# Kernel optimization log

Measured on AMD Instinct MI355X. Metric: run time of the kernel, lower is better.

## Reference

```python
import jax, jax.numpy as jnp
import numpy as np

B, S, D, H = 2, 2048, 2048, 16
HD = D // H
ROPE_BASE = 10000.0
N_DOCS = 8


def setup_inputs() -> dict:
    key = jax.random.key(0)
    ks = jax.random.split(key, 7)
    scale = 1.0 / np.sqrt(D)
    x = jax.random.normal(ks[0], (B, S, D), dtype=jnp.float32)
    doc_ids = jnp.sort(jax.random.randint(ks[1], (B, S), 0, N_DOCS), axis=1)
    Wq = jax.random.normal(ks[2], (D, D), dtype=jnp.float32) * scale
    Wk = jax.random.normal(ks[3], (D, D), dtype=jnp.float32) * scale
    Wv = jax.random.normal(ks[4], (D, D), dtype=jnp.float32) * scale
    Wo = jax.random.normal(ks[5], (D, D), dtype=jnp.float32) * scale
    bo = jax.random.normal(ks[6], (D,), dtype=jnp.float32) * 0.01
    return {"x": x, "doc_ids": doc_ids, "Wq": Wq, "Wk": Wk, "Wv": Wv, "Wo": Wo, "bo": bo}


def _rotate_half(t):
    # interleaved pairs: (x0,x1,x2,x3,...) -> (-x1,x0,-x3,x2,...)
    t1 = t[..., 0::2]
    t2 = t[..., 1::2]
    return jnp.stack((-t2, t1), axis=-1).reshape(t.shape)


def _doc_position_ids(doc_ids):
    b, s = doc_ids.shape
    boundary = jnp.concatenate(
        [jnp.ones((b, 1), dtype=bool), doc_ids[:, 1:] != doc_ids[:, :-1]], axis=1)
    ar = jnp.arange(s)[None, :]
    boundary_pos = jnp.where(boundary, ar, 0)
    last_boundary = jax.lax.cummax(boundary_pos, axis=1)
    return ar - last_boundary  # position within each document


def reference(x, doc_ids, Wq, Wk, Wv, Wo, bo):
    b, s, d = x.shape
    h, hd = H, HD

    q = (x @ Wq).reshape(b, s, h, hd).transpose(0, 2, 1, 3)  # [b,h,s,hd]
    k = (x @ Wk).reshape(b, s, h, hd).transpose(0, 2, 1, 3)
    v = (x @ Wv).reshape(b, s, h, hd).transpose(0, 2, 1, 3)

    # doc-aware RoPE: positions reset at document boundaries
    pos = _doc_position_ids(doc_ids).astype(jnp.float32)  # [b,s]
    inv_freq = 1.0 / (ROPE_BASE ** (jnp.arange(0, hd, 2, dtype=jnp.float32) / hd))
    freqs = pos[..., None] * inv_freq  # [b,s,hd/2]
    cos = jnp.repeat(jnp.cos(freqs), 2, axis=-1)[:, None]  # [b,1,s,hd]
    sin = jnp.repeat(jnp.sin(freqs), 2, axis=-1)[:, None]
    q = q * cos + _rotate_half(q) * sin
    k = k * cos + _rotate_half(k) * sin

    scores = jnp.einsum("bhqd,bhkd->bhqk", q, k)
    # doc-blockwise causal mask: attend only to j<=i within same document
    same_doc = doc_ids[:, :, None] == doc_ids[:, None, :]  # [b,s,s] (i,j)
    allowed = jnp.tril(same_doc)[:, None]  # [b,1,s,s]
    inv_scale = 1.0 / np.sqrt(hd)
    scores = jnp.where(allowed, scores * inv_scale, -jnp.inf)
    attn = jax.nn.softmax(scores, axis=-1)

    ctx = jnp.einsum("bhqk,bhkd->bhqd", attn, v)
    ctx = ctx.transpose(0, 2, 1, 3).reshape(b, s, d)
    return ctx @ Wo + bo
```

## Files before the change

### kernel.cpp

```cpp
#include <hip/hip_runtime.h>
#include <hip/hip_bf16.h>

#define Dd 2048
#define Ss 2048
#define Bb 2
#define Hh 16
#define HDd 128
#define BSs (Bb*Ss)
#define NTIL 32

typedef __bf16 bf16;
typedef __bf16 bf16x8 __attribute__((ext_vector_type(8)));
typedef __bf16 bf16x4 __attribute__((ext_vector_type(4)));
typedef float f32x4 __attribute__((ext_vector_type(4)));

__device__ __forceinline__ void gload_lds16(const void* g, void* l) {
  __builtin_amdgcn_global_load_lds((__attribute__((address_space(1))) void*)(g),
                                   (__attribute__((address_space(3))) void*)(l), 16, 0, 0);
}

template <int N>
__device__ __forceinline__ void waitv() {
  if constexpr (N == 0) asm volatile("s_waitcnt vmcnt(0)" ::: "memory");
  else if constexpr (N == 6) asm volatile("s_waitcnt vmcnt(6)" ::: "memory");
}

__global__ void k_cvtx(const float* __restrict__ x, bf16* __restrict__ xb) {
  int i = (blockIdx.x * 256 + threadIdx.x) * 4;
  f32x4 v = *(const f32x4*)(x + i);
  bf16x4 o;
  o[0] = (bf16)v[0]; o[1] = (bf16)v[1]; o[2] = (bf16)v[2]; o[3] = (bf16)v[3];
  *(bf16x4*)(xb + i) = o;
}

__global__ void k_tw(const float* __restrict__ W0, const float* __restrict__ W1,
                     const float* __restrict__ W2, const float* __restrict__ W3,
                     bf16* __restrict__ T0, bf16* __restrict__ T1,
                     bf16* __restrict__ T2, bf16* __restrict__ T3) {
  const float* W; bf16* T;
  switch (blockIdx.z) {
    case 0: W = W0; T = T0; break;
    case 1: W = W1; T = T1; break;
    case 2: W = W2; T = T2; break;
    default: W = W3; T = T3; break;
  }
  __shared__ float t[64][65];
  int n0 = blockIdx.x * 64, k0 = blockIdx.y * 64;
  int tid = threadIdx.x;
#pragma unroll
  for (int rr = 0; rr < 4; rr++) {
    int r = (tid >> 4) + rr * 16;
    f32x4 vv = *(const f32x4*)(W + (size_t)(k0 + r) * Dd + n0 + (tid & 15) * 4);
#pragma unroll
    for (int j = 0; j < 4; j++) t[r][(tid & 15) * 4 + j] = vv[j];
  }
  __syncthreads();
#pragma unroll
  for (int rr = 0; rr < 4; rr++) {
    int n = rr * 16 + (tid >> 4);
    int kb = (tid & 15) * 4;
    bf16x4 o;
#pragma unroll
    for (int j = 0; j < 4; j++) o[j] = (bf16)t[kb + j][n];
    *(bf16x4*)(T + (size_t)(n0 + n) * Dd + k0 + kb) = o;
  }
}

__global__ void k_pos(const int* __restrict__ doc, int* __restrict__ pos) {
  int b = blockIdx.x;
  __shared__ int bp[2][Ss];
  const int* db = doc + (size_t)b * Ss;
  for (int i = threadIdx.x; i < Ss; i += 1024) {
    int bd = (i == 0) || (db[i] != db[i - 1]);
    bp[0][i] = bd ? i : 0;
  }
  __syncthreads();
  int src = 0;
  for (int off = 1; off < Ss; off <<= 1) {
    for (int i = threadIdx.x; i < Ss; i += 1024) {
      int v = bp[src][i];
      if (i >= off) v = max(v, bp[src][i - off]);
      bp[1 - src][i] = v;
    }
    __syncthreads();
    src = 1 - src;
  }
  for (int i = threadIdx.x; i < Ss; i += 1024)
    pos[(size_t)b * Ss + i] = i - bp[src][i];
}

__device__ __forceinline__ void stage64(const char* gA, const char* gB,
                                        int m0, int n0, int t, int buf,
                                        char* AL, char* BL, int tid) {
  int ktb = t * 128;
#pragma unroll
  for (int p = 0; p < 2; p++) {
    int o = p * 8192 + tid * 16;
    int r = o >> 7, cb = o & 127;
    gload_lds16(gA + (size_t)(m0 + r) * 4096 + ktb + (cb ^ ((r & 7) << 4)),
                AL + buf * 16384 + o);
  }
#pragma unroll
  for (int p = 0; p < 4; p++) {
    int o = p * 8192 + tid * 16;
    int r = o >> 7, cb = o & 127;
    gload_lds16(gB + (size_t)(n0 + r) * 4096 + ktb + (cb ^ ((r & 7) << 4)),
                BL + buf * 32768 + o);
  }
}

template <bool STAGE, int WV>
__device__ __forceinline__ void do_tile64(const char* gA, const char* gB, int m0, int n0,
                                          int t, int bi, int b2, char* AL, char* BL, int tid,
                                          int wr, int wc, int ln, int g,
                                          f32x4 (&acc)[4][4]) {
  if (STAGE) stage64(gA, gB, m0, n0, t + 2, b2, AL, BL, tid);
  const char* tA = AL + bi * 16384;
  const char* tB = BL + bi * 32768;
#pragma unroll
  for (int kk = 0; kk < 2; kk++) {
    bf16x8 af[4], bf[4];
#pragma unroll
    for (int mq = 0; mq < 4; mq++) {
      int row = wr * 64 + mq * 16 + ln;
      af[mq] = *(const bf16x8*)(tA + row * 128 + ((kk * 64 + g * 16) ^ ((row & 7) << 4)));
    }
#pragma unroll
    for (int nq = 0; nq < 4; nq++) {
      int row = wc * 64 + nq * 16 + ln;
      bf[nq] = *(const bf16x8*)(tB + row * 128 + ((kk * 64 + g * 16) ^ ((row & 7) << 4)));
    }
    __builtin_amdgcn_s_setprio(1);
#pragma unroll
    for (int mq = 0; mq < 4; mq++)
#pragma unroll
      for (int nq = 0; nq < 4; nq++)
        acc[mq][nq] = __builtin_amdgcn_mfma_f32_16x16x32_bf16(af[mq], bf[nq], acc[mq][nq], 0, 0, 0);
    __builtin_amdgcn_s_setprio(0);
  }
  waitv<WV>();
  __builtin_amdgcn_s_barrier();
}

__device__ __forceinline__ void gemm64_core(const bf16* gA_, const bf16* gB_,
                                            int m0, int n0, char* AL, char* BL,
                                            f32x4 (&acc)[4][4]) {
  const char* gA = (const char*)gA_;
  const char* gB = (const char*)gB_;
  const int tid = threadIdx.x;
  const int l = tid & 63, w = tid >> 6;
  const int wr = w >> 2, wc = w & 3;
  const int g = l >> 4, ln = l & 15;
  f32x4 z = {0.f, 0.f, 0.f, 0.f};
#pragma unroll
  for (int i = 0; i < 4; i++)
#pragma unroll
    for (int n = 0; n < 4; n++) acc[i][n] = z;

  stage64(gA, gB, m0, n0, 0, 0, AL, BL, tid);
  stage64(gA, gB, m0, n0, 1, 1, AL, BL, tid);
  waitv<6>();
  __builtin_amdgcn_s_barrier();

  for (int tt = 0; tt < 10; tt++) {
    int t = tt * 3;
    do_tile64<true, 6>(gA, gB, m0, n0, t,     0, 2, AL, BL, tid, wr, wc, ln, g, acc);
    do_tile64<true, 6>(gA, gB, m0, n0, t + 1, 1, 0, AL, BL, tid, wr, wc, ln, g, acc);
    do_tile64<true, 6>(gA, gB, m0, n0, t + 2, 2, 1, AL, BL, tid, wr, wc, ln, g, acc);
  }
  do_tile64<false, 0>(gA, gB, m0, n0, 30, 0, 0, AL, BL, tid, wr, wc, ln, g, acc);
  do_tile64<false, -1>(gA, gB, m0, n0, 31, 1, 0, AL, BL, tid, wr, wc, ln, g, acc);
}

__global__ __launch_bounds__(512, 2) void k_qkv256(const bf16* __restrict__ xb,
                                                   const bf16* __restrict__ wqkvt,
                                                   const int* __restrict__ pos,
                                                   bf16* __restrict__ q,
                                                   bf16* __restrict__ k,
                                                   bf16* __restrict__ vt) {
  __shared__ char SLM[147456];
  char* AL = SLM;
  char* BL = SLM + 49152;
  int bid = blockIdx.x;
  int x = bid & 7, j = bid >> 3;
  int mt = j / 3, nt = x * 3 + (j % 3);
  int m0 = mt * 128, n0 = nt * 256;

  f32x4 acc[4][4];
  gemm64_core(xb, wqkvt, m0, n0, AL, BL, acc);

  const int tid = threadIdx.x;
  const int l = tid & 63, w = tid >> 6;
  const int wr = w >> 2, wc = w & 3, g = l >> 4, ln = l & 15;
  int z = n0 >> 11;
  int n0l = n0 & 2047;
  int bix = m0 >> 11;
  int sl0 = m0 & 2047;

  if (z == 2) {
#pragma unroll
    for (int mq = 0; mq < 4; mq++) {
      int sl = sl0 + wr * 64 + mq * 16 + g * 4;
#pragma unroll
      for (int nq = 0; nq < 4; nq++) {
        int col = n0l + wc * 64 + nq * 16 + ln;
        int h = col >> 7, hd = col & 127;
        bf16x4 o;
#pragma unroll
        for (int r2 = 0; r2 < 4; r2++) o[r2] = (bf16)acc[mq][nq][r2];
        *(bf16x4*)(vt + (((size_t)(bix * Hh + h) * HDd + hd) * Ss + sl)) = o;
      }
    }
  } else {
    bf16* dst = (z == 0) ? q : k;
    float* T = (float*)SLM;
    const float c1 = 0.14391156642398168f;
    int cg = (tid & 31) * 8;
    int hb = n0l + cg;
    int hh = hb >> 7, hd0 = hb & 127;
    float fr[4];
#pragma unroll
    for (int pr = 0; pr < 4; pr++)
      fr[pr] = __expf(-(float)((hd0 >> 1) + pr) * c1);

#pragma unroll
    for (int pass = 0; pass < 2; pass++) {
      __syncthreads();
      if (wr == pass) {
#pragma unroll
        for (int mq = 0; mq < 4; mq++) {
#pragma unroll
          for (int nq = 0; nq < 4; nq++) {
            int c = wc * 64 + nq * 16 + ln;
            int rb = mq * 16 + g * 4;
#pragma unroll
            for (int r2 = 0; r2 < 4; r2++)
              T[(rb + r2) * 260 + c] = acc[mq][nq][r2];
          }
        }
      }
      __syncthreads();
#pragma unroll
      for (int j2 = 0; j2 < 4; j2++) {
        int r = j2 * 16 + (tid >> 5);
        int sg = m0 + pass * 64 + r;
        float p = (float)pos[sg];
        f32x4 v0 = *(const f32x4*)(T + r * 260 + cg);
        f32x4 v1 = *(const f32x4*)(T + r * 260 + cg + 4);
        float e0[4] = {v0[0], v0[2], v1[0], v1[2]};
        float e1[4] = {v0[1], v0[3], v1[1], v1[3]};
        int s = sg & 2047;
        bf16x8 o;
#pragma unroll
        for (int pr = 0; pr < 4; pr++) {
          float ang = p * fr[pr];
          float sn, cs;
          __sincosf(ang, &sn, &cs);
          o[2 * pr]     = (bf16)(e0[pr] * cs - e1[pr] * sn);
          o[2 * pr + 1] = (bf16)(e1[pr] * cs + e0[pr] * sn);
        }
        *(bf16x8*)(dst + (((size_t)(bix * Hh + hh) * Ss + s) * HDd + hd0)) = o;
      }
    }
  }
}

__global__ __launch_bounds__(512, 2) void k_out256(const bf16* __restrict__ ctx,
                                                   const bf16* __restrict__ wot,
                                                   const float* __restrict__ bo,
                                                   float* __restrict__ outp) {
  __shared__ char AL[49152];
  __shared__ char BL[98304];
  int bid = blockIdx.x;
  int x = bid & 7, j = bid >> 3;
  int mt = j, nt = x;
  int m0 = mt * 128, n0 = nt * 256;

  f32x4 acc[4][4];
  gemm64_core(ctx, wot, m0, n0, AL, BL, acc);

  const int l = threadIdx.x & 63, w = threadIdx.x >> 6;
  const int wr = w >> 2, wc = w & 3, g = l >> 4, ln = l & 15;
  float bov[4];
#pragma unroll
  for (int nq = 0; nq < 4; nq++)
    bov[nq] = bo[n0 + wc * 64 + nq * 16 + ln];
#pragma unroll
  for (int mq = 0; mq < 4; mq++)
#pragma unroll
    for (int r2 = 0; r2 < 4; r2++) {
      int row = m0 + wr * 64 + mq * 16 + g * 4 + r2;
#pragma unroll
      for (int nq = 0; nq < 4; nq++) {
        int col = n0 + wc * 64 + nq * 16 + ln;
        outp[(size_t)row * Dd + col] = acc[mq][nq][r2] + bov[nq];
      }
    }
}

__global__ __launch_bounds__(256) void k_attn(const bf16* __restrict__ q,
                                              const bf16* __restrict__ k,
                                              const bf16* __restrict__ vt,
                                              const int* __restrict__ pos,
                                              bf16* __restrict__ ctx) {
  __shared__ bf16 Ks[64 * 128];
  __shared__ bf16 Vts[128 * 64];
  __shared__ bf16 Pw[4][16 * 64];
  int bid = blockIdx.x;
  int xc = bid & 7, jj = bid >> 3;
  int bh = xc * 4 + (jj >> 5);
  int qt = jj & 31;
  int b = bh >> 4, h = bh & 15;
  int q0 = qt * 64;
  const int tid = threadIdx.x, l = tid & 63, w = tid >> 6, g = l >> 4, ln = l & 15;
  const bf16* qb = q + (size_t)bh * Ss * HDd;
  const bf16* kb = k + (size_t)bh * Ss * HDd;
  const bf16* vb = vt + (size_t)bh * Ss * HDd;

  bf16x8 qf[4];
  int qr = q0 + w * 16 + ln;
#pragma unroll
  for (int ks = 0; ks < 4; ks++)
    qf[ks] = *(const bf16x8*)(qb + (size_t)qr * HDd + ks * 32 + 8 * g);

  int rrow[4], dstart[4];
  float m[4], lsum[4];
#pragma unroll
  for (int r2 = 0; r2 < 4; r2++) {
    rrow[r2] = q0 + w * 16 + 4 * g + r2;
    dstart[r2] = rrow[r2] - pos[(size_t)b * Ss + rrow[r2]];
    m[r2] = -1e30f;
    lsum[r2] = 0.f;
  }
  f32x4 oacc[8];
  f32x4 z = {0.f, 0.f, 0.f, 0.f};
#pragma unroll
  for (int n = 0; n < 8; n++) oacc[n] = z;

  int kt_start = (q0 - pos[(size_t)b * Ss + q0]) >> 6;
  const float iscale = 0.08838834764831845f;

  for (int kt = kt_start; kt <= qt; kt++) {
    int kv0 = kt * 64;
#pragma unroll
    for (int i2 = 0; i2 < 4; i2++) {
      int o = i2 * 4096 + w * 1024 + l * 16;
      int rk = o >> 8, cbk = o & 255;
      gload_lds16((const char*)kb + (size_t)(kv0 + rk) * 256 + cbk,
                  (char*)Ks + i2 * 4096 + w * 1024);
      int rv = o >> 7, cbv = o & 127;
      gload_lds16((const char*)vb + (size_t)rv * (Ss * 2) + (size_t)kv0 * 2 + cbv,
                  (char*)Vts + i2 * 4096 + w * 1024);
    }
    __syncthreads();

    f32x4 sc[4];
#pragma unroll
    for (int n = 0; n < 4; n++) {
      f32x4 a = z;
#pragma unroll
      for (int ks = 0; ks < 4; ks++) {
        bf16x8 bfrag = *(const bf16x8*)(Ks + (n * 16 + ln) * 128 + ks * 32 + 8 * g);
        a = __builtin_amdgcn_mfma_f32_16x16x32_bf16(qf[ks], bfrag, a, 0, 0, 0);
      }
      sc[n] = a;
    }

    float pmax[4] = {-1e30f, -1e30f, -1e30f, -1e30f};
    float pv[4][4];
#pragma unroll
    for (int n = 0; n < 4; n++) {
      int kvc = kv0 + n * 16 + ln;
#pragma unroll
      for (int r2 = 0; r2 < 4; r2++) {
        bool ok = (kvc <= rrow[r2]) && (kvc >= dstart[r2]);
        float sv = ok ? sc[n][r2] * iscale : -1e30f;
        pv[n][r2] = sv;
        pmax[r2] = fmaxf(pmax[r2], sv);
      }
    }
#pragma unroll
    for (int off = 1; off < 16; off <<= 1)
#pragma unroll
      for (int r2 = 0; r2 < 4; r2++)
        pmax[r2] = fmaxf(pmax[r2], __shfl_xor(pmax[r2], off, 64));

    float alpha[4];
#pragma unroll
    for (int r2 = 0; r2 < 4; r2++) {
      float mn = fmaxf(m[r2], pmax[r2]);
      alpha[r2] = __expf(m[r2] - mn);
      m[r2] = mn;
    }

    float rs[4] = {0.f, 0.f, 0.f, 0.f};
#pragma unroll
    for (int n = 0; n < 4; n++) {
      int kvc = kv0 + n * 16 + ln;
#pragma unroll
      for (int r2 = 0; r2 < 4; r2++) {
        bool ok = (kvc <= rrow[r2]) && (kvc >= dstart[r2]);
        float p = ok ? __expf(pv[n][r2] - m[r2]) : 0.f;
        rs[r2] += p;
        Pw[w][(4 * g + r2) * 64 + n * 16 + ln] = (bf16)p;
      }
    }
#pragma unroll
    for (int off = 1; off < 16; off <<= 1)
#pragma unroll
      for (int r2 = 0; r2 < 4; r2++) rs[r2] += __shfl_xor(rs[r2], off, 64);
#pragma unroll
    for (int r2 = 0; r2 < 4; r2++) lsum[r2] = lsum[r2] * alpha[r2] + rs[r2];
#pragma unroll
    for (int n = 0; n < 8; n++)
#pragma unroll
      for (int r2 = 0; r2 < 4; r2++) oacc[n][r2] *= alpha[r2];
    __syncthreads();

#pragma unroll
    for (int n = 0; n < 8; n++) {
#pragma unroll
      for (int ks = 0; ks < 2; ks++) {
        bf16x8 pa = *(const bf16x8*)(&Pw[w][ln * 64 + ks * 32 + 8 * g]);
        bf16x8 vfr = *(const bf16x8*)(Vts + (n * 16 + ln) * 64 + ks * 32 + 8 * g);
        oacc[n] = __builtin_amdgcn_mfma_f32_16x16x32_bf16(pa, vfr, oacc[n], 0, 0, 0);
      }
    }
    __syncthreads();
  }

#pragma unroll
  for (int n = 0; n < 8; n++)
#pragma unroll
    for (int r2 = 0; r2 < 4; r2++) {
      float val = oacc[n][r2] / lsum[r2];
      ctx[((size_t)(b * Ss + rrow[r2])) * Dd + h * HDd + n * 16 + ln] = (bf16)val;
    }
}

extern "C" void kernel_launch(void* const* d_in, const int* in_sizes, int n_in,
                              void* d_out, int out_size, void* d_ws, size_t ws_size,
                              hipStream_t stream) {
  const float* x = (const float*)d_in[0];
  const int* doc = (const int*)d_in[1];
  const float* Wq = (const float*)d_in[2];
  const float* Wk = (const float*)d_in[3];
  const float* Wv = (const float*)d_in[4];
  const float* Wo = (const float*)d_in[5];
  const float* bo = (const float*)d_in[6];
  float* outp = (float*)d_out;

  char* ws = (char*)d_ws;
  size_t off = 0;
  auto alloc = [&](size_t bytes) {
    char* p = ws + off;
    off += (bytes + 255) & ~(size_t)255;
    return p;
  };
  bf16* xb = (bf16*)alloc((size_t)BSs * Dd * 2);
  bf16* wqkvt = (bf16*)alloc((size_t)3 * Dd * Dd * 2);
  bf16* wot = (bf16*)alloc((size_t)Dd * Dd * 2);
  bf16* qd = (bf16*)alloc((size_t)BSs * Dd * 2);
  bf16* kd = (bf16*)alloc((size_t)BSs * Dd * 2);
  bf16* vtd = (bf16*)alloc((size_t)BSs * Dd * 2);
  bf16* ctxd = (bf16*)alloc((size_t)BSs * Dd * 2);
  int* pos = (int*)alloc((size_t)BSs * 4);

  k_cvtx<<<(BSs * Dd) / 1024, 256, 0, stream>>>(x, xb);
  k_tw<<<dim3(Dd / 64, Dd / 64, 4), 256, 0, stream>>>(
      Wq, Wk, Wv, Wo, wqkvt, wqkvt + (size_t)Dd * Dd, wqkvt + (size_t)2 * Dd * Dd, wot);
  k_pos<<<Bb, 1024, 0, stream>>>(doc, pos);
  k_qkv256<<<dim3(768), 512, 0, stream>>>(xb, wqkvt, pos, qd, kd, vtd);
  k_attn<<<dim3(1024), 256, 0, stream>>>(qd, kd, vtd, pos, ctxd);
  k_out256<<<dim3(256), 512, 0, stream>>>(ctxd, wot, bo, outp);
}
```

Baseline: 220.3 us.

## Use 256x384 per-head QKV GEMM tiles with interleaved weight layout

```diff
diff --git a/kernel.cpp b/kernel.cpp
--- a/kernel.cpp
+++ b/kernel.cpp
@@ -33,19 +33,15 @@
   *(bf16x4*)(xb + i) = o;
 }
 
-__global__ void k_tw(const float* __restrict__ W0, const float* __restrict__ W1,
-                     const float* __restrict__ W2, const float* __restrict__ W3,
-                     bf16* __restrict__ T0, bf16* __restrict__ T1,
-                     bf16* __restrict__ T2, bf16* __restrict__ T3) {
-  const float* W; bf16* T;
-  switch (blockIdx.z) {
-    case 0: W = W0; T = T0; break;
-    case 1: W = W1; T = T1; break;
-    case 2: W = W2; T = T2; break;
-    default: W = W3; T = T3; break;
-  }
+__global__ void k_tw(const float* __restrict__ Wq, const float* __restrict__ Wk,
+                     const float* __restrict__ Wv, const float* __restrict__ Wo,
+                     bf16* __restrict__ wqkvt, bf16* __restrict__ wot) {
+  int zz = blockIdx.z;
+  const float* W = (zz == 0) ? Wq : (zz == 1) ? Wk : (zz == 2) ? Wv : Wo;
+  bf16* T = (zz < 3) ? wqkvt : wot;
   __shared__ float t[64][65];
   int n0 = blockIdx.x * 64, k0 = blockIdx.y * 64;
+  int trow0 = (zz < 3) ? ((n0 >> 7) * 384 + zz * 128 + (n0 & 127)) : n0;
   int tid = threadIdx.x;
 #pragma unroll
   for (int rr = 0; rr < 4; rr++) {
@@ -62,7 +58,7 @@
     bf16x4 o;
 #pragma unroll
     for (int j = 0; j < 4; j++) o[j] = (bf16)t[kb + j][n];
-    *(bf16x4*)(T + (size_t)(n0 + n) * Dd + k0 + kb) = o;
+    *(bf16x4*)(T + (size_t)(trow0 + n) * Dd + k0 + kb) = o;
   }
 }
 
@@ -87,6 +83,175 @@
   }
   for (int i = threadIdx.x; i < Ss; i += 1024)
     pos[(size_t)b * Ss + i] = i - bp[src][i];
+}
+
+__device__ __forceinline__ void stage384(const char* gA, const char* gB,
+                                         int m0, int n0, int t, int buf,
+                                         char* AL, char* BL, int tid) {
+  int ktb = t * 128;
+#pragma unroll
+  for (int p = 0; p < 4; p++) {
+    int o = p * 8192 + tid * 16;
+    int r = o >> 7, cb = o & 127;
+    gload_lds16(gA + (size_t)(m0 + r) * 4096 + ktb + (cb ^ ((r & 7) << 4)),
+                AL + buf * 32768 + o);
+  }
+#pragma unroll
+  for (int p = 0; p < 6; p++) {
+    int o = p * 8192 + tid * 16;
+    int r = o >> 7, cb = o & 127;
+    gload_lds16(gB + (size_t)(n0 + r) * 4096 + ktb + (cb ^ ((r & 7) << 4)),
+                BL + buf * 49152 + o);
+  }
+}
+
+template <bool STAGE, int WV>
+__device__ __forceinline__ void do_tile384(const char* gA, const char* gB, int m0, int n0,
+                                           int t, int bi, char* AL, char* BL, int tid,
+                                           int wr, int wc, int ln, int g,
+                                           f32x4 (&acc)[8][6]) {
+  if (STAGE) stage384(gA, gB, m0, n0, t + 1, bi ^ 1, AL, BL, tid);
+  const char* tA = AL + bi * 32768;
+  const char* tB = BL + bi * 49152;
+#pragma unroll
+  for (int kk = 0; kk < 2; kk++) {
+    bf16x8 bf[6];
+#pragma unroll
+    for (int nq = 0; nq < 6; nq++) {
+      int row = wc * 96 + nq * 16 + ln;
+      bf[nq] = *(const bf16x8*)(tB + row * 128 + ((kk * 64 + g * 16) ^ ((row & 7) << 4)));
+    }
+#pragma unroll
+    for (int mh = 0; mh < 2; mh++) {
+      bf16x8 af[4];
+#pragma unroll
+      for (int mq = 0; mq < 4; mq++) {
+        int row = wr * 128 + mh * 64 + mq * 16 + ln;
+        af[mq] = *(const bf16x8*)(tA + row * 128 + ((kk * 64 + g * 16) ^ ((row & 7) << 4)));
+      }
+      __builtin_amdgcn_s_setprio(1);
+#pragma unroll
+      for (int mq = 0; mq < 4; mq++)
+#pragma unroll
+        for (int nq = 0; nq < 6; nq++)
+          acc[mh * 4 + mq][nq] =
+              __builtin_amdgcn_mfma_f32_16x16x32_bf16(af[mq], bf[nq], acc[mh * 4 + mq][nq], 0, 0, 0);
+      __builtin_amdgcn_s_setprio(0);
+    }
+  }
+  waitv<WV>();
+  if (WV >= 0) __builtin_amdgcn_s_barrier();
+}
+
+__global__ __launch_bounds__(512, 2) void k_qkv384(const bf16* __restrict__ xb,
+                                                   const bf16* __restrict__ wqkvt,
+                                                   const int* __restrict__ pos,
+                                                   bf16* __restrict__ q,
+                                                   bf16* __restrict__ k,
+                                                   bf16* __restrict__ vt) {
+  __shared__ char SLM[163840];
+  char* AL = SLM;
+  char* BL = SLM + 65536;
+  int bid = blockIdx.x;
+  int x = bid & 7, j = bid >> 3;
+  int nt = x * 2 + (j >> 4);
+  int mt = j & 15;
+  int m0 = mt * 256, n0 = nt * 384;
+
+  const int tid = threadIdx.x;
+  const int l = tid & 63, w = tid >> 6;
+  const int wr = w >> 2, wc = w & 3;
+  const int g = l >> 4, ln = l & 15;
+
+  f32x4 acc[8][6];
+  f32x4 z = {0.f, 0.f, 0.f, 0.f};
+#pragma unroll
+  for (int i = 0; i < 8; i++)
+#pragma unroll
+    for (int n = 0; n < 6; n++) acc[i][n] = z;
+
+  const char* gA = (const char*)xb;
+  const char* gB = (const char*)wqkvt;
+  stage384(gA, gB, m0, n0, 0, 0, AL, BL, tid);
+  waitv<0>();
+  __builtin_amdgcn_s_barrier();
+  for (int t = 0; t < NTIL - 1; t++)
+    do_tile384<true, 0>(gA, gB, m0, n0, t, t & 1, AL, BL, tid, wr, wc, ln, g, acc);
+  do_tile384<false, -1>(gA, gB, m0, n0, NTIL - 1, (NTIL - 1) & 1, AL, BL, tid, wr, wc, ln, g, acc);
+
+  int h = nt;
+  int bix = m0 >> 11;
+  int sl0 = m0 & 2047;
+
+#pragma unroll
+  for (int mq = 0; mq < 8; mq++) {
+    int sl = sl0 + wr * 128 + mq * 16 + g * 4;
+#pragma unroll
+    for (int nq = 0; nq < 6; nq++) {
+      int cb0 = wc * 96 + nq * 16;
+      if (cb0 >= 256) {
+        int hd = cb0 - 256 + ln;
+        bf16x4 o;
+#pragma unroll
+        for (int r2 = 0; r2 < 4; r2++) o[r2] = (bf16)acc[mq][nq][r2];
+        *(bf16x4*)(vt + (((size_t)(bix * Hh + h) * HDd + hd) * Ss + sl)) = o;
+      }
+    }
+  }
+
+  float* T = (float*)SLM;
+  const float c1 = 0.14391156642398168f;
+  int cg = (tid & 31) * 8;
+  int zz = cg >> 7;
+  int hd0 = cg & 127;
+  bf16* dst = (zz == 0) ? q : k;
+  float fr[4];
+#pragma unroll
+  for (int pr = 0; pr < 4; pr++)
+    fr[pr] = __expf(-(float)((hd0 >> 1) + pr) * c1);
+
+#pragma unroll
+  for (int pass = 0; pass < 4; pass++) {
+    __syncthreads();
+    if (wr == (pass >> 1)) {
+#pragma unroll
+      for (int mq2 = 0; mq2 < 4; mq2++) {
+        int mq = (pass & 1) * 4 + mq2;
+#pragma unroll
+        for (int nq = 0; nq < 6; nq++) {
+          int cb0 = wc * 96 + nq * 16;
+          if (cb0 < 256) {
+            int rb = mq2 * 16 + g * 4;
+#pragma unroll
+            for (int r2 = 0; r2 < 4; r2++)
+              T[(rb + r2) * 260 + cb0 + ln] = acc[mq][nq][r2];
+          }
+        }
+      }
+    }
+    __syncthreads();
+#pragma unroll
+    for (int j2 = 0; j2 < 4; j2++) {
+      int r = j2 * 16 + (tid >> 5);
+      int sg = m0 + pass * 64 + r;
+      float p = (float)pos[sg];
+      f32x4 v0 = *(const f32x4*)(T + r * 260 + cg);
+      f32x4 v1 = *(const f32x4*)(T + r * 260 + cg + 4);
+      float e0[4] = {v0[0], v0[2], v1[0], v1[2]};
+      float e1[4] = {v0[1], v0[3], v1[1], v1[3]};
+      int s = sg & 2047;
+      bf16x8 o;
+#pragma unroll
+      for (int pr = 0; pr < 4; pr++) {
+        float ang = p * fr[pr];
+        float sn, cs;
+        __sincosf(ang, &sn, &cs);
+        o[2 * pr]     = (bf16)(e0[pr] * cs - e1[pr] * sn);
+        o[2 * pr + 1] = (bf16)(e1[pr] * cs + e0[pr] * sn);
+      }
+      *(bf16x8*)(dst + (((size_t)(bix * Hh + h) * Ss + s) * HDd + hd0)) = o;
+    }
+  }
 }
 
 __device__ __forceinline__ void stage64(const char* gA, const char* gB,
@@ -170,99 +335,6 @@
   }
   do_tile64<false, 0>(gA, gB, m0, n0, 30, 0, 0, AL, BL, tid, wr, wc, ln, g, acc);
   do_tile64<false, -1>(gA, gB, m0, n0, 31, 1, 0, AL, BL, tid, wr, wc, ln, g, acc);
-}
-
-__global__ __launch_bounds__(512, 2) void k_qkv256(const bf16* __restrict__ xb,
-                                                   const bf16* __restrict__ wqkvt,
-                                                   const int* __restrict__ pos,
-                                                   bf16* __restrict__ q,
-                                                   bf16* __restrict__ k,
-                                                   bf16* __restrict__ vt) {
-  __shared__ char SLM[147456];
-  char* AL = SLM;
-  char* BL = SLM + 49152;
-  int bid = blockIdx.x;
-  int x = bid & 7, j = bid >> 3;
-  int mt = j / 3, nt = x * 3 + (j % 3);
-  int m0 = mt * 128, n0 = nt * 256;
-
-  f32x4 acc[4][4];
-  gemm64_core(xb, wqkvt, m0, n0, AL, BL, acc);
-
-  const int tid = threadIdx.x;
-  const int l = tid & 63, w = tid >> 6;
-  const int wr = w >> 2, wc = w & 3, g = l >> 4, ln = l & 15;
-  int z = n0 >> 11;
-  int n0l = n0 & 2047;
-  int bix = m0 >> 11;
-  int sl0 = m0 & 2047;
-
-  if (z == 2) {
-#pragma unroll
-    for (int mq = 0; mq < 4; mq++) {
-      int sl = sl0 + wr * 64 + mq * 16 + g * 4;
-#pragma unroll
-      for (int nq = 0; nq < 4; nq++) {
-        int col = n0l + wc * 64 + nq * 16 + ln;
-        int h = col >> 7, hd = col & 127;
-        bf16x4 o;
-#pragma unroll
-        for (int r2 = 0; r2 < 4; r2++) o[r2] = (bf16)acc[mq][nq][r2];
-        *(bf16x4*)(vt + (((size_t)(bix * Hh + h) * HDd + hd) * Ss + sl)) = o;
-      }
-    }
-  } else {
-    bf16* dst = (z == 0) ? q : k;
-    float* T = (float*)SLM;
-    const float c1 = 0.14391156642398168f;
-    int cg = (tid & 31) * 8;
-    int hb = n0l + cg;
-    int hh = hb >> 7, hd0 = hb & 127;
-    float fr[4];
-#pragma unroll
-    for (int pr = 0; pr < 4; pr++)
-      fr[pr] = __expf(-(float)((hd0 >> 1) + pr) * c1);
-
-#pragma unroll
-    for (int pass = 0; pass < 2; pass++) {
-      __syncthreads();
-      if (wr == pass) {
-#pragma unroll
-        for (int mq = 0; mq < 4; mq++) {
-#pragma unroll
-          for (int nq = 0; nq < 4; nq++) {
-            int c = wc * 64 + nq * 16 + ln;
-            int rb = mq * 16 + g * 4;
-#pragma unroll
-            for (int r2 = 0; r2 < 4; r2++)
-              T[(rb + r2) * 260 + c] = acc[mq][nq][r2];
-          }
-        }
-      }
-      __syncthreads();
-#pragma unroll
-      for (int j2 = 0; j2 < 4; j2++) {
-        int r = j2 * 16 + (tid >> 5);
-        int sg = m0 + pass * 64 + r;
-        float p = (float)pos[sg];
-        f32x4 v0 = *(const f32x4*)(T + r * 260 + cg);
-        f32x4 v1 = *(const f32x4*)(T + r * 260 + cg + 4);
-        float e0[4] = {v0[0], v0[2], v1[0], v1[2]};
-        float e1[4] = {v0[1], v0[3], v1[1], v1[3]};
-        int s = sg & 2047;
-        bf16x8 o;
-#pragma unroll
-        for (int pr = 0; pr < 4; pr++) {
-          float ang = p * fr[pr];
-          float sn, cs;
-          __sincosf(ang, &sn, &cs);
-          o[2 * pr]     = (bf16)(e0[pr] * cs - e1[pr] * sn);
-          o[2 * pr + 1] = (bf16)(e1[pr] * cs + e0[pr] * sn);
-        }
-        *(bf16x8*)(dst + (((size_t)(bix * Hh + hh) * Ss + s) * HDd + hd0)) = o;
-      }
-    }
-  }
 }
 
 __global__ __launch_bounds__(512, 2) void k_out256(const bf16* __restrict__ ctx,
@@ -467,10 +539,9 @@
   int* pos = (int*)alloc((size_t)BSs * 4);
 
   k_cvtx<<<(BSs * Dd) / 1024, 256, 0, stream>>>(x, xb);
-  k_tw<<<dim3(Dd / 64, Dd / 64, 4), 256, 0, stream>>>(
-      Wq, Wk, Wv, Wo, wqkvt, wqkvt + (size_t)Dd * Dd, wqkvt + (size_t)2 * Dd * Dd, wot);
+  k_tw<<<dim3(Dd / 64, Dd / 64, 4), 256, 0, stream>>>(Wq, Wk, Wv, Wo, wqkvt, wot);
   k_pos<<<Bb, 1024, 0, stream>>>(doc, pos);
-  k_qkv256<<<dim3(768), 512, 0, stream>>>(xb, wqkvt, pos, qd, kd, vtd);
+  k_qkv384<<<dim3(256), 512, 0, stream>>>(xb, wqkvt, pos, qd, kd, vtd);
   k_attn<<<dim3(1024), 256, 0, stream>>>(qd, kd, vtd, pos, ctxd);
   k_out256<<<dim3(256), 512, 0, stream>>>(ctxd, wot, bo, outp);
 }
```

New measurement: 225.6 us. +2.4%, slower.
